# Kernel optimization log

Hardware: AMD Instinct MI355X
Metric: run time of the kernel (lower is better)

The kernel has to match this reference:

```python
import jax, jax.numpy as jnp
import numpy as np

N, B, E, H, D, L, NT = 30000, 16, 60000, 128, 64, 2, 5


def _build_graph():
    rng = np.random.default_rng(0)
    ng = N // B
    row = rng.integers(0, N, size=E)
    g = row // ng
    col = g * ng + rng.integers(0, ng, size=E)  # bonds stay within a graph
    order = np.argsort(g, kind='stable')        # sort bonds by graph id
    row, col = row[order], col[order]
    edge_index = np.stack([row, col]).astype(np.int32)
    # bond graph: bonds adjacent iff they share an atom (vectorized _build_bond_graph)
    atoms = np.concatenate([row, col])
    bonds = np.concatenate([np.arange(E), np.arange(E)])
    o2 = np.argsort(atoms, kind='stable')
    sb = bonds[o2]
    counts = np.bincount(atoms, minlength=N)
    offs = np.concatenate([[0], np.cumsum(counts)[:-1]])
    sq = counts * counts
    total = int(sq.sum())
    gid = np.repeat(np.arange(N), sq)
    poff = np.concatenate([[0], np.cumsum(sq)[:-1]])
    pos = np.arange(total) - np.repeat(poff, sq)
    c, o = counts[gid], offs[gid]
    ii, jj = pos // c, pos % c
    mask = ii != jj
    bond_edge_index = np.stack([sb[o + ii][mask], sb[o + jj][mask]]).astype(np.int32)
    batch = np.repeat(np.arange(B), ng).astype(np.int32)
    return edge_index, bond_edge_index, batch


def setup_inputs() -> dict:
    edge_index, bond_edge_index, batch = _build_graph()
    key = jax.random.key(0)
    ks = jax.random.split(key, 16)
    s = 0.05
    n = lambda k, shp: jax.random.normal(k, shp, jnp.float32) * s
    return {
        'atom_features': jax.random.normal(ks[0], (N, H), jnp.float32),
        'atom_pos': jax.random.normal(ks[1], (N, 3), jnp.float32),
        'atomic_numbers': jax.random.randint(ks[2], (N,), 1, 20, jnp.int32),
        'batch': jnp.asarray(batch),
        'edge_index': jnp.asarray(edge_index),
        'bond_edge_index': jnp.asarray(bond_edge_index),
        'iw1': n(ks[3], (2 * H, D)), 'ib1': jnp.zeros((D,), jnp.float32),
        'iw2': n(ks[4], (D, D)), 'ib2': jnp.zeros((D,), jnp.float32),
        'emb': n(ks[5], (L, NT, D)),
        'mw1': n(ks[6], (L, 3 * D, D)), 'mb1': jnp.zeros((L, D), jnp.float32),
        'mw2': n(ks[7], (L, D, D)), 'mb2': jnp.zeros((L, D), jnp.float32),
        'uw1': n(ks[8], (L, 2 * D, D)), 'ub1': jnp.zeros((L, D), jnp.float32),
        'uw2': n(ks[9], (L, D, D)), 'ub2': jnp.zeros((L, D), jnp.float32),
        'num_graphs': B,
    }


def reference(atom_features, atom_pos, iw1, ib1, iw2, ib2, emb, mw1, mb1, mw2, mb2,
              uw1, ub1, uw2, ub2, atomic_numbers, batch, edge_index, bond_edge_index,
              num_graphs):
    row, col = edge_index
    hi, hj = atom_features[row], atom_features[col]  # [E, H] gathers
    # bond_init MLP
    x = jax.nn.silu(jnp.concatenate([hi, hj], -1) @ iw1 + ib1) @ iw2 + ib2  # [E, D]
    # _classify_bonds: cosine-similarity thresholds (order matters, matches torch)
    ni = jnp.maximum(jnp.linalg.norm(hi, axis=-1), 1e-8)
    nj = jnp.maximum(jnp.linalg.norm(hj, axis=-1), 1e-8)
    sim = jnp.sum(hi * hj, -1) / (ni * nj)
    bt = jnp.where(sim > 0.8, 1, 0)
    bt = jnp.where(sim > 0.9, 2, bt)
    bt = jnp.where(sim < 0.3, 3, bt)
    src, dst = bond_edge_index  # x_j = x[src], x_i = x[dst]; aggregate at dst
    nb = x.shape[0]
    deg = jax.ops.segment_sum(jnp.ones(src.shape, jnp.float32), dst, num_segments=nb)
    denom = jnp.maximum(deg, 1.0)[:, None]  # PyG mean aggr: 0 for isolated nodes
    for l in range(mw1.shape[0]):
        te = emb[l][bt]  # [E, D] bond-type embedding
        msg_in = jnp.concatenate([x[dst], x[src], te[dst]], -1)  # [BE, 3D]
        msg = jax.nn.silu(msg_in @ mw1[l] + mb1[l]) @ mw2[l] + mb2[l]
        aggr = jax.ops.segment_sum(msg, dst, num_segments=nb) / denom
        upd_in = jnp.concatenate([aggr, x], -1)
        x = x + jax.nn.silu(upd_in @ uw1[l] + ub1[l]) @ uw2[l] + ub2[l]
    # pooling: edges are sorted by graph, so repeat_interleave == batch[row]
    bond_batch = batch[row]
    cnt = jax.ops.segment_sum(jnp.ones((nb,), jnp.float32), bond_batch, num_segments=num_graphs)
    gfeat = jax.ops.segment_sum(x, bond_batch, num_segments=num_graphs) / jnp.maximum(cnt, 1.0)[:, None]
    return x, gfeat
```

## Files before the change

kernel.cpp:

```cpp
#include <hip/hip_runtime.h>
#include <hip/hip_cooperative_groups.h>
#include <cstdint>
#include <cstddef>

namespace cg = cooperative_groups;

#define HDIM 128
#define DDIM 64
#define NTYPES 5
#define NGRAPHS 16
#define EPB 64
#define SCAP 1024
#define PREPB 132

typedef __attribute__((ext_vector_type(8))) short short8;
typedef __attribute__((ext_vector_type(4))) float f32x4;

static __device__ __forceinline__ short8 as_s8(uint4 u) {
    return __builtin_bit_cast(short8, u);
}

static __device__ __forceinline__ float silu_f(float v) {
    return v * __builtin_amdgcn_rcpf(1.0f + __expf(-v));
}
// ... 221 lines not shown
    const float* __restrict__ emb, const float* __restrict__ mw1,
    const float* __restrict__ mb1, const float* __restrict__ mw2,
    const float* __restrict__ mb2, const float* __restrict__ uw1,
    const float* __restrict__ uw2, const float* __restrict__ iw2,
    const float* __restrict__ iw1,
    float* __restrict__ tt, float* __restrict__ b2u,
    uint4* __restrict__ fw2u, uint4* __restrict__ fu1b, uint4* __restrict__ fu2,
    uint4* __restrict__ fp, uint4* __restrict__ fiw2, uint4* __restrict__ fp0,
    uint4* __restrict__ fiw1, int* __restrict__ cnt, int E) {
    for (int i = blockIdx.x * 256 + threadIdx.x; i < E; i += gridDim.x * 256)
        cnt[i] = 0;
    if (threadIdx.x < 64)
        dev_prep(blockIdx.x, threadIdx.x, emb, mw1, mb1, mw2, mb2, uw1, uw2, iw2, iw1,
                 tt, b2u, fw2u, fu1b, fu2, fp, fiw2, fp0, fiw1);
}

static __device__ __forceinline__ int slotIdx(int row, int slot) {
    return row * 8 + (slot ^ (row & 7));
}
static __device__ __forceinline__ int slotIdx16(int row, int slot) {
    return row * 16 + (slot ^ (row & 7));
}

static __device__ __forceinline__ short8 ldFragA(const uint4* buf, int rowBase, int lane, int ks) {
    int row = rowBase + (lane & 15);
    int slot = ks * 4 + (lane >> 4);
    return as_s8(buf[slotIdx(row, slot)]);
}
static __device__ __forceinline__ short8 ldFragA16(const uint4* buf, int rowBase, int lane, int slot0) {
    int row = rowBase + (lane & 15);
    int slot = slot0 + (lane >> 4);
    return as_s8(buf[slotIdx16(row, slot)]);
}

static __device__ __forceinline__ void loadB(const uint4* __restrict__ frag, int jt, int lane,
                                             short8& h0, short8& h1, short8& l0, short8& l1) {
    const uint4* p0 = frag + ((size_t)(jt * 2 + 0) * 64 + lane) * 2;
    const uint4* p1 = frag + ((size_t)(jt * 2 + 1) * 64 + lane) * 2;
    h0 = as_s8(p0[0]); l0 = as_s8(p0[1]);
    h1 = as_s8(p1[0]); l1 = as_s8(p1[1]);
}

static __device__ __forceinline__ f32x4 gemm_tile(const uint4* Ahi, const uint4* Alo,
        int rowBase, int lane,
        short8 bh0, short8 bh1, short8 bl0, short8 bl1, f32x4 acc) {
    short8 ah0 = ldFragA(Ahi, rowBase, lane, 0);
    short8 ah1 = ldFragA(Ahi, rowBase, lane, 1);
    short8 al0 = ldFragA(Alo, rowBase, lane, 0);
    short8 al1 = ldFragA(Alo, rowBase, lane, 1);
    acc = __builtin_amdgcn_mfma_f32_16x16x32_bf16(ah0, bh0, acc, 0, 0, 0);
    acc = __builtin_amdgcn_mfma_f32_16x16x32_bf16(ah1, bh1, acc, 0, 0, 0);
    acc = __builtin_amdgcn_mfma_f32_16x16x32_bf16(al0, bh0, acc, 0, 0, 0);
    acc = __builtin_amdgcn_mfma_f32_16x16x32_bf16(al1, bh1, acc, 0, 0, 0);
    acc = __builtin_amdgcn_mfma_f32_16x16x32_bf16(ah0, bl0, acc, 0, 0, 0);
    acc = __builtin_amdgcn_mfma_f32_16x16x32_bf16(ah1, bl1, acc, 0, 0, 0);
    return acc;
}

static __device__ __forceinline__ f32x4 gemm_tile16(const uint4* Ahi, const uint4* Alo,
        int rowBase, int lane, int sb,
        short8 bh0, short8 bh1, short8 bl0, short8 bl1, f32x4 acc) {
    short8 ah0 = ldFragA16(Ahi, rowBase, lane, sb + 0);
    short8 ah1 = ldFragA16(Ahi, rowBase, lane, sb + 4);
    short8 al0 = ldFragA16(Alo, rowBase, lane, sb + 0);
    short8 al1 = ldFragA16(Alo, rowBase, lane, sb + 4);
    acc = __builtin_amdgcn_mfma_f32_16x16x32_bf16(ah0, bh0, acc, 0, 0, 0);
    acc = __builtin_amdgcn_mfma_f32_16x16x32_bf16(ah1, bh1, acc, 0, 0, 0);
    acc = __builtin_amdgcn_mfma_f32_16x16x32_bf16(al0, bh0, acc, 0, 0, 0);
    acc = __builtin_amdgcn_mfma_f32_16x16x32_bf16(al1, bh1, acc, 0, 0, 0);
    acc = __builtin_amdgcn_mfma_f32_16x16x32_bf16(ah0, bl0, acc, 0, 0, 0);
    acc = __builtin_amdgcn_mfma_f32_16x16x32_bf16(ah1, bl1, acc, 0, 0, 0);
    return acc;
}

static __device__ __forceinline__ void dev_atom_proj(
    int a0, int tid, int lane, int w,
    const float* __restrict__ AF, const uint4* __restrict__ fIw1,
    float* __restrict__ pa, float* __restrict__ qa, float* __restrict__ na, int N,
    uint4* sHi, uint4* sLo) {
    {
        int dl = tid >> 3, q = tid & 7;
        int a = a0 + dl;
        bool ok = a < N;
        const float* ar = AF + (size_t)(ok ? a : 0) * HDIM + q * 16;
        float4 v0 = ld4(ar + 0), v1 = ld4(ar + 4), v2 = ld4(ar + 8), v3 = ld4(ar + 12);
        float nrm = v0.x*v0.x + v0.y*v0.y + v0.z*v0.z + v0.w*v0.w
                  + v1.x*v1.x + v1.y*v1.y + v1.z*v1.z + v1.w*v1.w
                  + v2.x*v2.x + v2.y*v2.y + v2.z*v2.z + v2.w*v2.w
                  + v3.x*v3.x + v3.y*v3.y + v3.z*v3.z + v3.w*v3.w;
        nrm += __shfl_xor(nrm, 1, 64);
        nrm += __shfl_xor(nrm, 2, 64);
        nrm += __shfl_xor(nrm, 4, 64);
        if (q == 0 && ok) na[a] = sqrtf(nrm);
        float f0[8] = {v0.x, v0.y, v0.z, v0.w, v1.x, v1.y, v1.z, v1.w};
        float f1[8] = {v2.x, v2.y, v2.z, v2.w, v3.x, v3.y, v3.z, v3.w};
        if (!ok) {
            #pragma unroll
            for (int i = 0; i < 8; ++i) { f0[i] = 0.f; f1[i] = 0.f; }
        }
        uint4 h, l;
        hilo8(f0, h, l);
        int s0 = slotIdx16(dl, q * 2);
        sHi[s0] = h; sLo[s0] = l;
        hilo8(f1, h, l);
        int s1 = slotIdx16(dl, q * 2 + 1);
        sHi[s1] = h; sLo[s1] = l;
    }
    int jt = w & 3;
    const uint4* m0 = fIw1 + ((w < 4) ? 0 : 2048);
    short8 B0h0, B0h1, B0l0, B0l1, B1h0, B1h1, B1l0, B1l1;
    loadB(m0, jt, lane, B0h0, B0h1, B0l0, B0l1);
    loadB(m0 + 1024, jt, lane, B1h0, B1h1, B1l0, B1l1);
    __syncthreads();

    float* dst = (w < 4) ? pa : qa;
    int j = jt * 16 + (lane & 15);
    f32x4 z4 = {0.f, 0.f, 0.f, 0.f};
    #pragma unroll
    for (int rt = 0; rt < 4; ++rt) {
        f32x4 acc = gemm_tile16(sHi, sLo, rt * 16, lane, 0, B0h0, B0h1, B0l0, B0l1, z4);
        acc = gemm_tile16(sHi, sLo, rt * 16, lane, 8, B1h0, B1h1, B1l0, B1l1, acc);
        #pragma unroll
        for (int r = 0; r < 4; ++r) {
            int rowi = rt * 16 + (lane >> 4) * 4 + r;
            int a = a0 + rowi;
            if (a < N) dst[(size_t)a * DDIM + j] = acc[r];
        }
    }
}

__global__ void __launch_bounds__(512) atom_proj_k(
    const float* __restrict__ AF, const uint4* __restrict__ fIw1,
    float* __restrict__ pa, float* __restrict__ qa, float* __restrict__ na, int N) {
    __shared__ uint4 sHi[1024];
    __shared__ uint4 sLo[1024];
    int tid = threadIdx.x, lane = tid & 63;
    int w = __builtin_amdgcn_readfirstlane((int)(tid >> 6));
    int a0 = blockIdx.x * 64;
    if (a0 < N)
        dev_atom_proj(a0, tid, lane, w, AF, fIw1, pa, qa, na, N, sHi, sLo);
}

static __device__ __forceinline__ void dev_bond_init(
    int lb, int tid, int lane, int w,
    const float* __restrict__ AF, const int* __restrict__ row, const int* __restrict__ col,
    const float* __restrict__ pa, const float* __restrict__ qa, const float* __restrict__ na,
    const float* __restrict__ b1, const uint4* __restrict__ fW2, const float* __restrict__ b2,
    const uint4* __restrict__ fP0,
    float* __restrict__ x, int* __restrict__ bt,
    float* __restrict__ pd, uint4* __restrict__ ps, int E,
    uint4* sAhi, uint4* sAlo, uint4* sXhi, uint4* sXlo, bool storeX) {
    int e0 = lb * EPB;

    {
        int dl = tid >> 3, q = tid & 7;
        int d = e0 + dl;
        bool ok = d < E;
        int dd = ok ? d : 0;
        int r = row[dd], c = col[dd];
        int jq = q * 8;

        const float* hi = AF + (size_t)r * HDIM + q * 16;
        const float* hj = AF + (size_t)c * HDIM + q * 16;
        float dt = 0.f;
        #pragma unroll
        for (int k = 0; k < 16; k += 4) {
            float4 a4 = ld4(hi + k), b4 = ld4(hj + k);
            dt += a4.x * b4.x + a4.y * b4.y + a4.z * b4.z + a4.w * b4.w;
        }
        dt += __shfl_xor(dt, 1, 64);
        dt += __shfl_xor(dt, 2, 64);
        dt += __shfl_xor(dt, 4, 64);
        if (q == 0 && ok) {
            float nr = fmaxf(na[r], 1e-8f), nc = fmaxf(na[c], 1e-8f);
            float sim = dt / (nr * nc);
            int t = 0;
            if (sim > 0.8f) t = 1;
            if (sim > 0.9f) t = 2;
            if (sim < 0.3f) t = 3;
            bt[d] = t;
        }

        const float* pr = pa + (size_t)r * DDIM + jq;
        const float* qc = qa + (size_t)c * DDIM + jq;
        float4 p0 = ld4(pr + 0), p1 = ld4(pr + 4);
        float4 q0 = ld4(qc + 0), q1 = ld4(qc + 4);
        float hv[8];
        hv[0] = silu_f(p0.x + q0.x + b1[jq + 0]);
        hv[1] = silu_f(p0.y + q0.y + b1[jq + 1]);
        hv[2] = silu_f(p0.z + q0.z + b1[jq + 2]);
        hv[3] = silu_f(p0.w + q0.w + b1[jq + 3]);
        hv[4] = silu_f(p1.x + q1.x + b1[jq + 4]);
        hv[5] = silu_f(p1.y + q1.y + b1[jq + 5]);
        hv[6] = silu_f(p1.z + q1.z + b1[jq + 6]);
        hv[7] = silu_f(p1.w + q1.w + b1[jq + 7]);
        if (!ok) {
            #pragma unroll
            for (int i = 0; i < 8; ++i) hv[i] = 0.f;
        }
        uint4 h4, l4;
        hilo8(hv, h4, l4);
        int si = slotIdx(dl, q);
        sAhi[si] = h4; sAlo[si] = l4;
    }
    int jt = w & 3, mh = w >> 2;
    short8 W2h0, W2h1, W2l0, W2l1;
    loadB(fW2, jt, lane, W2h0, W2h1, W2l0, W2l1);
    __syncthreads();

    int rb0 = mh * 32, rb1 = mh * 32 + 16;
    f32x4 z4 = {0.f, 0.f, 0.f, 0.f};
    f32x4 acc0 = gemm_tile(sAhi, sAlo, rb0, lane, W2h0, W2h1, W2l0, W2l1, z4);
    f32x4 acc1 = gemm_tile(sAhi, sAlo, rb1, lane, W2h0, W2h1, W2l0, W2l1, z4);
    int j = jt * 16 + (lane & 15);
    float b2j = b2[j];
    unsigned short* hX = (unsigned short*)sXhi;
    unsigned short* lX = (unsigned short*)sXlo;
    #pragma unroll
    for (int r = 0; r < 4; ++r) {
        int rowi = rb0 + (lane >> 4) * 4 + r;
        int e = e0 + rowi;
        float xn = acc0[r] + b2j;
        if (storeX && e < E) x[(size_t)e * DDIM + j] = xn;
        unsigned int hb = bf16r(xn);
        float lov = xn - __uint_as_float(hb << 16);
        int ui = (rowi * 8 + ((j >> 3) ^ (rowi & 7))) * 8 + (j & 7);
        hX[ui] = (unsigned short)hb;
        lX[ui] = (unsigned short)bf16r(lov);
    }
    #pragma unroll
    for (int r = 0; r < 4; ++r) {
        int rowi = rb1 + (lane >> 4) * 4 + r;
        int e = e0 + rowi;
        float xn = acc1[r] + b2j;
        if (storeX && e < E) x[(size_t)e * DDIM + j] = xn;
        unsigned int hb = bf16r(xn);
        float lov = xn - __uint_as_float(hb << 16);
        int ui = (rowi * 8 + ((j >> 3) ^ (rowi & 7))) * 8 + (j & 7);
        hX[ui] = (unsigned short)hb;
        lX[ui] = (unsigned short)bf16r(lov);
    }
    __syncthreads();

    const uint4* fPw = (w < 4) ? fP0 : (fP0 + 1024);
    int jp = w & 3;
    short8 Ph0, Ph1, Pl0, Pl1;
    loadB(fPw, jp, lane, Ph0, Ph1, Pl0, Pl1);
    f32x4 q0 = gemm_tile(sXhi, sXlo, 0,  lane, Ph0, Ph1, Pl0, Pl1, z4);
    f32x4 q1 = gemm_tile(sXhi, sXlo, 16, lane, Ph0, Ph1, Pl0, Pl1, z4);
    f32x4 q2 = gemm_tile(sXhi, sXlo, 32, lane, Ph0, Ph1, Pl0, Pl1, z4);
    f32x4 q3 = gemm_tile(sXhi, sXlo, 48, lane, Ph0, Ph1, Pl0, Pl1, z4);
    unsigned short* hA = (unsigned short*)sAhi;
    if (w < 4) {
        int jd = jp * 16 + (lane & 15);
        #pragma unroll
        for (int mt = 0; mt < 4; ++mt) {
            f32x4 qq = (mt == 0) ? q0 : (mt == 1) ? q1 : (mt == 2) ? q2 : q3;
            #pragma unroll
            for (int r = 0; r < 4; ++r) {
                int rowi = mt * 16 + (lane >> 4) * 4 + r;
                int e = e0 + rowi;
                if (e < E) pd[(size_t)e * DDIM + jd] = qq[r];
            }
        }
    } else {
        int js = jp * 16 + (lane & 15);
        #pragma unroll
        for (int mt = 0; mt < 4; ++mt) {
            f32x4 qq = (mt == 0) ? q0 : (mt == 1) ? q1 : (mt == 2) ? q2 : q3;
            #pragma unroll
            for (int r = 0; r < 4; ++r) {
                int rowi = mt * 16 + (lane >> 4) * 4 + r;
                int ui = (rowi * 8 + ((js >> 3) ^ (rowi & 7))) * 8 + (js & 7);
                hA[ui] = (unsigned short)bf16r(qq[r]);
            }
        }
    }
    __syncthreads();
    {
        int dl = tid >> 3, q = tid & 7;
        int d = e0 + dl;
        if (d < E) ps[(size_t)d * 8 + q] = sAhi[slotIdx(dl, q)];
    }
}

__global__ void __launch_bounds__(512, 4) bond_init2_k(
    const float* __restrict__ AF, const int* __restrict__ row, const int* __restrict__ col,
    const float* __restrict__ pa, const float* __restrict__ qa, const float* __restrict__ na,
    const float* __restrict__ b1, const uint4* __restrict__ fW2, const float* __restrict__ b2,
    const uint4* __restrict__ fP0,
    float* __restrict__ x, int* __restrict__ bt,
    float* __restrict__ pd, uint4* __restrict__ ps, int E) {
    __shared__ uint4 sAhi[512];
    __shared__ uint4 sAlo[512];
    __shared__ uint4 sXhi[512];
    __shared__ uint4 sXlo[512];
    int nEB = (E + EPB - 1) / EPB;
    int lb = xcd_logical_block();
    if (lb >= nEB) return;
    int tid = threadIdx.x, lane = tid & 63;
    int w = __builtin_amdgcn_readfirstlane((int)(tid >> 6));
    dev_bond_init(lb, tid, lane, w, AF, row, col, pa, qa, na, b1, fW2, b2, fP0,
                  x, bt, pd, ps, E, sAhi, sAlo, sXhi, sXlo, true);
}

__global__ void __launch_bounds__(256) proj_k(const float* __restrict__ x,
                                              const float* __restrict__ w1 ,
                                              float* __restrict__ pd, uint4* __restrict__ ps,
                                              int E) {
    int lane = threadIdx.x & 63;
    int w = __builtin_amdgcn_readfirstlane((int)(threadIdx.x >> 6));
    int e = blockIdx.x * EPB + lane;
    bool ok = e < E;
    int eidx = ok ? e : 0;
    int j0 = w * 16;
    const float* xr = x + (size_t)eidx * DDIM;

    float apd[16], aps[16];
    #pragma unroll
    for (int jj = 0; jj < 16; ++jj) { apd[jj] = 0.f; aps[jj] = 0.f; }
    #pragma unroll 2
    for (int c = 0; c < 16; ++c) {
        float4 v = ld4(xr + c * 4);
        float xv[4] = {v.x, v.y, v.z, v.w};
        #pragma unroll
        for (int kk = 0; kk < 4; ++kk) {
            int k = c * 4 + kk;
            const float* wd = w1 + (size_t)k * DDIM + j0;
            const float* wsv = w1 + (size_t)(DDIM + k) * DDIM + j0;
            #pragma unroll
            for (int jj = 0; jj < 16; ++jj) {
                apd[jj] = fmaf(xv[kk], wd[jj], apd[jj]);
                aps[jj] = fmaf(xv[kk], wsv[jj], aps[jj]);
            }
        }
    }
    if (ok) {
        float* pr = pd + (size_t)e * DDIM + j0;
        st4(pr + 0,  make_float4(apd[0],  apd[1],  apd[2],  apd[3]));
        st4(pr + 4,  make_float4(apd[4],  apd[5],  apd[6],  apd[7]));
        st4(pr + 8,  make_float4(apd[8],  apd[9],  apd[10], apd[11]));
        st4(pr + 12, make_float4(apd[12], apd[13], apd[14], apd[15]));
        ps[(size_t)e * 8 + 2 * w + 0] = pack8(aps + 0);
        ps[(size_t)e * 8 + 2 * w + 1] = pack8(aps + 8);
    }
}

static __device__ __forceinline__ void dev_layer(
    int lb, int tid, int lane, int w,
    float* __restrict__ x, const float* __restrict__ pd, const uint4* __restrict__ ps,
    const float* __restrict__ tt_l, const int* __restrict__ bt,
    const int* __restrict__ offs, const int* __restrict__ srclist,
    const int* __restrict__ cnt,
    const uint4* __restrict__ fW2u, const float* __restrict__ b2u,
    const uint4* __restrict__ fU1b, const float* __restrict__ ub1,
    const uint4* __restrict__ fU2, const float* __restrict__ ub2,
    const uint4* __restrict__ fP, float* __restrict__ pdn, uint4* __restrict__ psn,
    int E, const int* __restrict__ erow, const int* __restrict__ gbatch,
    float* __restrict__ gfeat, int doPool,
    uint4* sAhi, uint4* sAlo, uint4* sXhi, uint4* sXlo,
    float* degLDS, int* gidLDS, int* sIdx, bool loadX, bool storeX3) {
    int e0 = lb * EPB;
    int pb0 = offs[e0];

    {
        int dl = tid >> 3, q = tid & 7;
        int d = e0 + dl;
        bool ok = d < E;
        int dd = ok ? d : 0;
        int jq = q * 8;
        float4 xv0 = make_float4(0, 0, 0, 0), xv1 = xv0;
        if (loadX) {
            const float* xr = x + (size_t)dd * DDIM + jq;
            xv0 = ld4(xr + 0); xv1 = ld4(xr + 4);
        }
        int dc = cnt[dd];
        int rAtom = (doPool && ok) ? erow[dd] : 0;
        const float* pr = pd + (size_t)dd * DDIM + jq;
        const float* tp = tt_l + (size_t)bt[dd] * DDIM + jq;
        float4 b0 = add4(ld4(pr + 0), ld4(tp + 0));
        float4 b1 = add4(ld4(pr + 4), ld4(tp + 4));
        int p0v = ok ? offs[d] : pb0, p1v = ok ? offs[d + 1] : pb0;

        int emax = min(e0 + EPB, E);
        int pT = offs[emax] - pb0;
        for (int i = tid; i < pT && i < SCAP; i += 512) sIdx[i] = srclist[pb0 + i];
        __syncthreads();

        float4 s0 = make_float4(0, 0, 0, 0), s1 = s0;
        if (p1v - pb0 <= SCAP) {
            int li = p0v - pb0, le = p1v - pb0;
            for (; li + 4 <= le; li += 4) {
                uint4 u0 = ps[(size_t)sIdx[li + 0] * 8 + q];
                uint4 u1 = ps[(size_t)sIdx[li + 1] * 8 + q];
                uint4 u2 = ps[(size_t)sIdx[li + 2] * 8 + q];
                uint4 u3 = ps[(size_t)sIdx[li + 3] * 8 + q];
                float4 a, b;
                unpack8(u0, a, b);
                silu_acc4(s0, add4(b0, a));
                silu_acc4(s1, add4(b1, b));
                unpack8(u1, a, b);
                silu_acc4(s0, add4(b0, a));
                silu_acc4(s1, add4(b1, b));
                unpack8(u2, a, b);
                silu_acc4(s0, add4(b0, a));
                silu_acc4(s1, add4(b1, b));
                unpack8(u3, a, b);
                silu_acc4(s0, add4(b0, a));
                silu_acc4(s1, add4(b1, b));
            }
            for (; li < le; ++li) {
                uint4 u0 = ps[(size_t)sIdx[li] * 8 + q];
                float4 a, b;
                unpack8(u0, a, b);
                silu_acc4(s0, add4(b0, a));
                silu_acc4(s1, add4(b1, b));
            }
        } else {
            int p = p0v;
            for (; p + 4 <= p1v; p += 4) {
                uint4 u0 = ps[(size_t)srclist[p + 0] * 8 + q];
                uint4 u1 = ps[(size_t)srclist[p + 1] * 8 + q];
                uint4 u2 = ps[(size_t)srclist[p + 2] * 8 + q];
                uint4 u3 = ps[(size_t)srclist[p + 3] * 8 + q];
                float4 a, b;
                unpack8(u0, a, b);
                silu_acc4(s0, add4(b0, a));
                silu_acc4(s1, add4(b1, b));
                unpack8(u1, a, b);
                silu_acc4(s0, add4(b0, a));
                silu_acc4(s1, add4(b1, b));
                unpack8(u2, a, b);
                silu_acc4(s0, add4(b0, a));
                silu_acc4(s1, add4(b1, b));
                unpack8(u3, a, b);
                silu_acc4(s0, add4(b0, a));
                silu_acc4(s1, add4(b1, b));
            }
            for (; p < p1v; ++p) {
                uint4 u0 = ps[(size_t)srclist[p] * 8 + q];
                float4 a, b;
                unpack8(u0, a, b);
                silu_acc4(s0, add4(b0, a));
                silu_acc4(s1, add4(b1, b));
            }
        }
        float inv = 1.0f / fmaxf((float)dc, 1.0f);
        float sv[8] = {s0.x * inv, s0.y * inv, s0.z * inv, s0.w * inv,
                       s1.x * inv, s1.y * inv, s1.z * inv, s1.w * inv};
        if (!ok) {
            #pragma unroll
            for (int i = 0; i < 8; ++i) sv[i] = 0.f;
        }
        uint4 h4, l4;
        int si = slotIdx(dl, q);
        hilo8(sv, h4, l4);
        sAhi[si] = h4; sAlo[si] = l4;
        if (loadX) {
            float xf[8] = {xv0.x, xv0.y, xv0.z, xv0.w, xv1.x, xv1.y, xv1.z, xv1.w};
            if (!ok) {
                #pragma unroll
                for (int i = 0; i < 8; ++i) xf[i] = 0.f;
            }
            hilo8(xf, h4, l4);
            sXhi[si] = h4; sXlo[si] = l4;
        }
        if (q == 0) {
            degLDS[dl] = (ok && dc > 0) ? 1.0f : 0.0f;
            gidLDS[dl] = (doPool && ok) ? gbatch[rAtom] : -1;
        }
    }
    int jt = w & 3, mh = w >> 2;
    short8 A2h0, A2h1, A2l0, A2l1;
    short8 U1h0, U1h1, U1l0, U1l1;
    loadB(fW2u, jt, lane, A2h0, A2h1, A2l0, A2l1);
    loadB(fU1b, jt, lane, U1h0, U1h1, U1l0, U1l1);
    __syncthreads();

    int rb0 = mh * 32, rb1 = mh * 32 + 16;
    f32x4 z4 = {0.f, 0.f, 0.f, 0.f};
    f32x4 acc0 = z4, acc1 = z4;
    acc0 = gemm_tile(sAhi, sAlo, rb0, lane, A2h0, A2h1, A2l0, A2l1, acc0);
    acc0 = gemm_tile(sXhi, sXlo, rb0, lane, U1h0, U1h1, U1l0, U1l1, acc0);
    acc1 = gemm_tile(sAhi, sAlo, rb1, lane, A2h0, A2h1, A2l0, A2l1, acc1);
    acc1 = gemm_tile(sXhi, sXlo, rb1, lane, U1h0, U1h1, U1l0, U1l1, acc1);
    __syncthreads();
    int j = jt * 16 + (lane & 15);
    float ub1j = ub1[j], b2uj = b2u[j];
    unsigned short* hA = (unsigned short*)sAhi;
    unsigned short* lA = (unsigned short*)sAlo;
    #pragma unroll
    for (int r = 0; r < 4; ++r) {
        int row = rb0 + (lane >> 4) * 4 + r;
        float hv = silu_f(acc0[r] + ub1j + degLDS[row] * b2uj);
        unsigned int hb = bf16r(hv);
        float lov = hv - __uint_as_float(hb << 16);
        int ui = (row * 8 + ((j >> 3) ^ (row & 7))) * 8 + (j & 7);
        hA[ui] = (unsigned short)hb;
        lA[ui] = (unsigned short)bf16r(lov);
    }
    #pragma unroll
    for (int r = 0; r < 4; ++r) {
        int row = rb1 + (lane >> 4) * 4 + r;
        float hv = silu_f(acc1[r] + ub1j + degLDS[row] * b2uj);
        unsigned int hb = bf16r(hv);
        float lov = hv - __uint_as_float(hb << 16);
        int ui = (row * 8 + ((j >> 3) ^ (row & 7))) * 8 + (j & 7);
        hA[ui] = (unsigned short)hb;
        lA[ui] = (unsigned short)bf16r(lov);
    }
    __syncthreads();

    short8 U2h0, U2h1, U2l0, U2l1;
    loadB(fU2, jt, lane, U2h0, U2h1, U2l0, U2l1);
    f32x4 o0 = gemm_tile(sAhi, sAlo, rb0, lane, U2h0, U2h1, U2l0, U2l1, z4);
    f32x4 o1 = gemm_tile(sAhi, sAlo, rb1, lane, U2h0, U2h1, U2l0, U2l1, z4);
    float ub2j = ub2[j];
    bool haveP = (fP != nullptr);
    unsigned short* hX = (unsigned short*)sXhi;
    unsigned short* lX = (unsigned short*)sXlo;
    float xnv0[4], xnv1[4];
    #pragma unroll
    for (int r = 0; r < 4; ++r) {
        int row = rb0 + (lane >> 4) * 4 + r;
        int e = e0 + row;
        int ui = (row * 8 + ((j >> 3) ^ (row & 7))) * 8 + (j & 7);
        float xvv = __uint_as_float((unsigned int)hX[ui] << 16)
                  + __uint_as_float((unsigned int)lX[ui] << 16);
        float xn = xvv + o0[r] + ub2j;
        xnv0[r] = xn;
        if (storeX3 && e < E) x[(size_t)e * DDIM + j] = xn;
        if (haveP) {
            unsigned int hb = bf16r(xn);
            float lov = xn - __uint_as_float(hb << 16);
            hX[ui] = (unsigned short)hb;
            lX[ui] = (unsigned short)bf16r(lov);
        }
    }
    #pragma unroll
    for (int r = 0; r < 4; ++r) {
        int row = rb1 + (lane >> 4) * 4 + r;
        int e = e0 + row;
        int ui = (row * 8 + ((j >> 3) ^ (row & 7))) * 8 + (j & 7);
        float xvv = __uint_as_float((unsigned int)hX[ui] << 16)
                  + __uint_as_float((unsigned int)lX[ui] << 16);
        float xn = xvv + o1[r] + ub2j;
        xnv1[r] = xn;
        if (storeX3 && e < E) x[(size_t)e * DDIM + j] = xn;
        if (haveP) {
            unsigned int hb = bf16r(xn);
            float lov = xn - __uint_as_float(hb << 16);
            hX[ui] = (unsigned short)hb;
            lX[ui] = (unsigned short)bf16r(lov);
        }
    }
    if (!haveP) {
        if (doPool) {
            __syncthreads();
            float* poolB = (float*)sAhi;
            if (tid < 256) poolB[tid] = 0.f;
            __syncthreads();
            int gid0 = gidLDS[0];
            bool uni = (gidLDS[EPB - 1] == gid0);
            if (uni) {
                float s = xnv0[0] + xnv0[1] + xnv0[2] + xnv0[3]
                        + xnv1[0] + xnv1[1] + xnv1[2] + xnv1[3];
                atomicAdd(&poolB[j], s);
            } else {
                #pragma unroll
                for (int r = 0; r < 4; ++r) {
                    int row = rb0 + (lane >> 4) * 4 + r;
                    int g = gidLDS[row];
                    if (g >= 0) {
                        int sl = g - gid0;
                        if (sl < 4) atomicAdd(&poolB[sl * DDIM + j], xnv0[r]);
                        else atomicAdd(&gfeat[(size_t)g * DDIM + j], xnv0[r]);
                    }
                }
                #pragma unroll
                for (int r = 0; r < 4; ++r) {
                    int row = rb1 + (lane >> 4) * 4 + r;
                    int g = gidLDS[row];
                    if (g >= 0) {
                        int sl = g - gid0;
                        if (sl < 4) atomicAdd(&poolB[sl * DDIM + j], xnv1[r]);
                        else atomicAdd(&gfeat[(size_t)g * DDIM + j], xnv1[r]);
                    }
                }
            }
            __syncthreads();
            if (tid < 256) {
                int sl = tid >> 6;
                int g = gid0 + sl;
                float v = poolB[tid];
                if (v != 0.f && g < NGRAPHS)
                    atomicAdd(&gfeat[(size_t)g * DDIM + (tid & 63)], v);
            }
        }
        return;
    }
    __syncthreads();

    const uint4* fPw = (w < 4) ? fP : (fP + 1024);
    int jp = w & 3;
    short8 Ph0, Ph1, Pl0, Pl1;
    loadB(fPw, jp, lane, Ph0, Ph1, Pl0, Pl1);
    f32x4 q0 = gemm_tile(sXhi, sXlo, 0,  lane, Ph0, Ph1, Pl0, Pl1, z4);
    f32x4 q1 = gemm_tile(sXhi, sXlo, 16, lane, Ph0, Ph1, Pl0, Pl1, z4);
    f32x4 q2 = gemm_tile(sXhi, sXlo, 32, lane, Ph0, Ph1, Pl0, Pl1, z4);
    f32x4 q3 = gemm_tile(sXhi, sXlo, 48, lane, Ph0, Ph1, Pl0, Pl1, z4);
    if (w < 4) {
        int jd = jp * 16 + (lane & 15);
        #pragma unroll
        for (int mt = 0; mt < 4; ++mt) {
            f32x4 qq = (mt == 0) ? q0 : (mt == 1) ? q1 : (mt == 2) ? q2 : q3;
            #pragma unroll
            for (int r = 0; r < 4; ++r) {
                int row = mt * 16 + (lane >> 4) * 4 + r;
                int e = e0 + row;
                if (e < E) pdn[(size_t)e * DDIM + jd] = qq[r];
            }
        }
    } else {
        int js = jp * 16 + (lane & 15);
        #pragma unroll
        for (int mt = 0; mt < 4; ++mt) {
            f32x4 qq = (mt == 0) ? q0 : (mt == 1) ? q1 : (mt == 2) ? q2 : q3;
            #pragma unroll
            for (int r = 0; r < 4; ++r) {
                int row = mt * 16 + (lane >> 4) * 4 + r;
                int ui = (row * 8 + ((js >> 3) ^ (row & 7))) * 8 + (js & 7);
                hA[ui] = (unsigned short)bf16r(qq[r]);
            }
        }
    }
    __syncthreads();
    {
        int dl = tid >> 3, q = tid & 7;
        int d = e0 + dl;
        if (d < E) psn[(size_t)d * 8 + q] = sAhi[slotIdx(dl, q)];
    }
}

__global__ void __launch_bounds__(512, 4) layer_k(
    float* __restrict__ x, const float* __restrict__ pd, const uint4* __restrict__ ps,
    const float* __restrict__ tt_l, const int* __restrict__ bt,
    const int* __restrict__ offs, const int* __restrict__ srclist,
    const int* __restrict__ cnt,
    const uint4* __restrict__ fW2u, const float* __restrict__ b2u,
    const uint4* __restrict__ fU1b, const float* __restrict__ ub1,
    const uint4* __restrict__ fU2, const float* __restrict__ ub2,
    const uint4* __restrict__ fP,
    float* __restrict__ pdn, uint4* __restrict__ psn, int E,
    const int* __restrict__ erow, const int* __restrict__ gbatch,
    float* __restrict__ gfeat, int doPool) {
    __shared__ uint4 sAhi[512];
    __shared__ uint4 sAlo[512];
    __shared__ uint4 sXhi[512];
    __shared__ uint4 sXlo[512];
    __shared__ float degLDS[64];
    __shared__ int   gidLDS[64];
    __shared__ int   sIdx[SCAP];
    int nEB = (E + EPB - 1) / EPB;
    int lb = xcd_logical_block();
    if (lb >= nEB) return;
    int tid = threadIdx.x, lane = tid & 63;
    int w = __builtin_amdgcn_readfirstlane((int)(tid >> 6));
    dev_layer(lb, tid, lane, w, x, pd, ps, tt_l, bt, offs, srclist, cnt,
              fW2u, b2u, fU1b, ub1, fU2, ub2, fP, pdn, psn, E,
              erow, gbatch, gfeat, doPool,
              sAhi, sAlo, sXhi, sXlo, degLDS, gidLDS, sIdx, true, true);
}

static __device__ __forceinline__ int lower_bound_bb(const int* __restrict__ row,
                                                     const int* __restrict__ batch,
                                                     int E, int g) {
    int lo = 0, hi = E;
    while (lo < hi) {
        int m = (lo + hi) >> 1;
        if (batch[row[m]] < g) lo = m + 1; else hi = m;
    }
    return lo;
}

__global__ void __launch_bounds__(64) pool_final_k(
    const int* __restrict__ row, const int* __restrict__ batch,
    float* __restrict__ gfeat, int E) {
    int g = blockIdx.x, j = threadIdx.x;
    int s = lower_bound_bb(row, batch, E, g);
    int t = lower_bound_bb(row, batch, E, g + 1);
    float cnt = fmaxf((float)(t - s), 1.0f);
    gfeat[g * DDIM + j] /= cnt;
}

__global__ void __launch_bounds__(512, 8) fused_k(
    float* x, const int* row, const int* col,
    const float* AF, const uint4* fIw1, float* pa, float* qa, float* na, int N,
    const float* ib1, const uint4* fIw2, const float* ib2, const uint4* fP0,
    int* bt, float* pd, uint4* ps,
    const float* tt, int* offs, int* srclist, int* cnt,
    const uint4* fW2u, const float* b2u, const uint4* fU1b, const float* ub1,
    const uint4* fU2, const float* ub2, const uint4* fP,
    float* pd2, uint4* ps2,
    const int* gbatch, float* gfeat, int E,
    const int* bsrc, const int* bdst, int BE,
    int* bsum, int* bpre, int* cursor) {
    __shared__ uint4 U1[1024];
    __shared__ uint4 U2[1024];
    __shared__ float degLDS[64];
    __shared__ int   gidLDS[64];
    __shared__ int   sIdx[SCAP];
    cg::grid_group grid = cg::this_grid();
    int tid = threadIdx.x, lane = tid & 63;
    int w = __builtin_amdgcn_readfirstlane((int)(tid >> 6));
    uint4* sAhi = U1;
    uint4* sAlo = U1 + 512;
    uint4* sXhi = U2;
    uint4* sXlo = U2 + 512;
    int nEB = (E + EPB - 1) / EPB;
    int lb = xcd_logical_block();

    if ((int)blockIdx.x * 64 < N)
        dev_atom_proj((int)blockIdx.x * 64, tid, lane, w, AF, fIw1, pa, qa, na, N, U1, U2);
    for (int i = (int)blockIdx.x * 512 + tid; i < BE; i += (int)gridDim.x * 512)
        __hip_atomic_fetch_add(&cnt[bdst[i]], 1, __ATOMIC_RELAXED, __HIP_MEMORY_SCOPE_AGENT);
    if (blockIdx.x == gridDim.x - 1)
        for (int i = tid; i < NGRAPHS * DDIM; i += 512) gfeat[i] = 0.f;
    __threadfence();
    grid.sync();

    if (lb < nEB) {
        dev_bond_init(lb, tid, lane, w, AF, row, col, pa, qa, na, ib1, fIw2, ib2, fP0,
                      x, bt, pd, ps, E, sAhi, sAlo, sXhi, sXlo, false);
        if (tid < 64) {
            int e = lb * EPB + tid;
            int v = (e < E) ? cnt[e] : 0;
            v += __shfl_xor(v, 1, 64);
            v += __shfl_xor(v, 2, 64);
            v += __shfl_xor(v, 4, 64);
            v += __shfl_xor(v, 8, 64);
            v += __shfl_xor(v, 16, 64);
            v += __shfl_xor(v, 32, 64);
            if (tid == 0) bsum[lb] = v;
        }
    }
    __threadfence();
    grid.sync();

    if (blockIdx.x == 0) {
        for (int i = tid; i < SCAP; i += 512) sIdx[i] = (i < nEB) ? bsum[i] : 0;
        __syncthreads();
        for (int off = 1; off < SCAP; off <<= 1) {
            int i2 = tid + 512;
            int v0 = (tid >= off) ? sIdx[tid - off] : 0;
            int v1 = sIdx[i2 - off];
            __syncthreads();
            sIdx[tid] += v0;
            sIdx[i2] += v1;
            __syncthreads();
        }
        for (int i = tid; i < nEB; i += 512) bpre[i] = sIdx[i] - bsum[i];
    }
    __threadfence();
    grid.sync();

    if (lb < nEB) {
        int e0 = lb * EPB;
        int myc = 0;
        if (tid < 64) {
            int e = e0 + tid;
            myc = (e < E) ? cnt[e] : 0;
            gidLDS[tid] = myc;
        }
        __syncthreads();
        for (int off = 1; off < 64; off <<= 1) {
            int v = 0;
            if (tid < 64 && tid >= off) v = gidLDS[tid - off];
            __syncthreads();
            if (tid < 64) gidLDS[tid] += v;
            __syncthreads();
        }
        if (tid < 64) {
            int e = e0 + tid;
            if (e < E) {
                int ex = gidLDS[tid] - myc + bpre[lb];
                offs[e] = ex;
                cursor[e] = ex;
                if (e == E - 1) offs[E] = ex + myc;
            }
        }
    }
    __threadfence();
    grid.sync();

    for (int i = (int)blockIdx.x * 512 + tid; i < BE; i += (int)gridDim.x * 512) {
        int d = bdst[i];
        int p = __hip_atomic_fetch_add(&cursor[d], 1, __ATOMIC_RELAXED,
                                       __HIP_MEMORY_SCOPE_AGENT);
        srclist[p] = bsrc[i];
    }
    __threadfence();
    grid.sync();

    if (lb < nEB)
        dev_layer(lb, tid, lane, w, x, pd, ps, tt, bt, offs, srclist, cnt,
                  fW2u, b2u, fU1b, ub1, fU2, ub2, fP, pd2, ps2, E,
                  row, gbatch, gfeat, 0,
                  sAhi, sAlo, sXhi, sXlo, degLDS, gidLDS, sIdx, false, false);
    __threadfence();
    grid.sync();

    if (lb < nEB)
        dev_layer(lb, tid, lane, w, x, pd2, ps2, tt + NTYPES * DDIM, bt, offs, srclist, cnt,
                  fW2u + 1024, b2u + DDIM, fU1b + 1024, ub1 + DDIM,
                  fU2 + 1024, ub2 + DDIM, nullptr, nullptr, nullptr, E,
                  row, gbatch, gfeat, 1,
                  sAhi, sAlo, sXhi, sXlo, degLDS, gidLDS, sIdx, false, true);
    __threadfence();
    grid.sync();

    if ((int)blockIdx.x < NGRAPHS && tid < 64) {
        int g = blockIdx.x, j = tid;
        int s = lower_bound_bb(row, gbatch, E, g);
        int t = lower_bound_bb(row, gbatch, E, g + 1);
        float c = fmaxf((float)(t - s), 1.0f);
        gfeat[g * DDIM + j] /= c;
    }
}

extern "C" void kernel_launch(void* const* d_in, const int* in_sizes, int n_in,
                              void* d_out, int out_size, void* d_ws, size_t ws_size,
                              hipStream_t stream) {
    (void)n_in; (void)out_size;
    const float* AF    = (const float*)d_in[0];
    const int*   batch = (const int*)d_in[3];
    const int*   edge_index      = (const int*)d_in[4];
    const int*   bond_edge_index = (const int*)d_in[5];
    const float* iw1 = (const float*)d_in[6];
    const float* ib1 = (const float*)d_in[7];
    const float* iw2 = (const float*)d_in[8];
    const float* ib2 = (const float*)d_in[9];
    const float* emb = (const float*)d_in[10];
    const float* mw1 = (const float*)d_in[11];
    const float* mb1 = (const float*)d_in[12];
    const float* mw2 = (const float*)d_in[13];
    const float* mb2 = (const float*)d_in[14];
    const float* uw1 = (const float*)d_in[15];
    const float* ub1 = (const float*)d_in[16];
    const float* uw2 = (const float*)d_in[17];
    const float* ub2 = (const float*)d_in[18];

    const int N  = in_sizes[0] / HDIM;
    const int E  = in_sizes[4] / 2;
    const int BE = in_sizes[5] / 2;
    const int NB = (E + 255) / 256;
    const int EB = (E + EPB - 1) / EPB;
    const int nEB = EB;
    const int APB = (N + 63) / 64;
    const int EBS = ((EB + 7) / 8) * 8;
    const int CNTB = (BE + 255) / 256;

    float* xout  = (float*)d_out;
    float* gfeat = xout + (size_t)E * DDIM;

    char* w = (char*)d_ws;
    float* tt       = (float*)w;  w += sizeof(float) * 2 * NTYPES * DDIM;
    float* b2u      = (float*)w;  w += sizeof(float) * 2 * DDIM;
    w = (char*)(((uintptr_t)w + 15) & ~(uintptr_t)15);
    uint4* fW2u     = (uint4*)w;  w += 2048 * sizeof(uint4);
    uint4* fU1b     = (uint4*)w;  w += 2048 * sizeof(uint4);
    uint4* fU2      = (uint4*)w;  w += 2048 * sizeof(uint4);
    uint4* fP       = (uint4*)w;  w += 2048 * sizeof(uint4);
    uint4* fIw2     = (uint4*)w;  w += 1024 * sizeof(uint4);
    uint4* fP0      = (uint4*)w;  w += 2048 * sizeof(uint4);
    uint4* fIw1     = (uint4*)w;  w += 4096 * sizeof(uint4);
    int*   cnt      = (int*)w;    w += sizeof(int) * E;
    int*   offs     = (int*)w;    w += sizeof(int) * (E + 1);
    int*   cursor   = (int*)w;    w += sizeof(int) * E;
    int*   bt       = (int*)w;    w += sizeof(int) * E;
    int*   srclist  = (int*)w;    w += sizeof(int) * BE;
    int*   bsum     = (int*)w;    w += sizeof(int) * 1024;
    int*   bpre     = (int*)w;    w += sizeof(int) * 1024;
    w = (char*)(((uintptr_t)w + 15) & ~(uintptr_t)15);
    float* pd       = (float*)w;  w += sizeof(float) * (size_t)E * DDIM;
    uint4* ps       = (uint4*)w;  w += sizeof(unsigned short) * (size_t)E * DDIM;
    float* pa       = (float*)w;  w += sizeof(float) * (size_t)N * DDIM;
    float* qa       = (float*)w;  w += sizeof(float) * (size_t)N * DDIM;
    float* na       = (float*)w;  w += sizeof(float) * (size_t)N;
    w = (char*)(((uintptr_t)w + 15) & ~(uintptr_t)15);
    float* pd2      = (float*)w;  w += sizeof(float) * (size_t)E * DDIM;
    uint4* ps2      = (uint4*)w;  w += sizeof(unsigned short) * (size_t)E * DDIM;
    bool fuse_proj = ((size_t)(w - (char*)d_ws) <= ws_size);

    const int* row  = edge_index;
    const int* col  = edge_index + E;
    const int* bsrc = bond_edge_index;
    const int* bdst = bond_edge_index + BE;

    prep_k<<<PREPB, 256, 0, stream>>>(emb, mw1, mb1, mw2, mb2, uw1, uw2, iw2, iw1,
                                      tt, b2u, fW2u, fU1b, fU2, fP, fIw2, fP0, fIw1,
                                      cnt, E);

    static int s_coopBlocks = -1;
    if (s_coopBlocks < 0) {
        int dev = 0;
        hipGetDevice(&dev);
        int coopAttr = 0;
        hipDeviceGetAttribute(&coopAttr, hipDeviceAttributeCooperativeLaunch, dev);
        int nCU = 0;
        hipDeviceGetAttribute(&nCU, hipDeviceAttributeMultiprocessorCount, dev);
        int mb = 0;
        hipError_t oe = hipOccupancyMaxActiveBlocksPerMultiprocessor(&mb, fused_k, 512, 0);
        s_coopBlocks = (coopAttr && oe == hipSuccess && nCU > 0) ? mb * nCU : 0;
    }

    bool coopDone = false;
    if (fuse_proj && s_coopBlocks >= EBS && nEB <= SCAP) {
        int Nv = N, Ev = E, BEv = BE;
        void* kargs[] = {
            (void*)&xout, (void*)&row, (void*)&col,
            (void*)&AF, (void*)&fIw1, (void*)&pa, (void*)&qa, (void*)&na, (void*)&Nv,
            (void*)&ib1, (void*)&fIw2, (void*)&ib2, (void*)&fP0,
            (void*)&bt, (void*)&pd, (void*)&ps,
            (void*)&tt, (void*)&offs, (void*)&srclist, (void*)&cnt,
            (void*)&fW2u, (void*)&b2u, (void*)&fU1b, (void*)&ub1,
            (void*)&fU2, (void*)&ub2, (void*)&fP,
            (void*)&pd2, (void*)&ps2,
            (void*)&batch, (void*)&gfeat, (void*)&Ev,
            (void*)&bsrc, (void*)&bdst, (void*)&BEv,
            (void*)&bsum, (void*)&bpre, (void*)&cursor };
        hipError_t le = hipLaunchCooperativeKernel((const void*)fused_k, dim3(EBS),
                                                   dim3(512), kargs, 0, stream);
        coopDone = (le == hipSuccess);
    }

    if (!coopDone) {
        count_k<<<CNTB, 256, 0, stream>>>(bdst, cnt, BE);
        bsum_k<<<NB, 256, 0, stream>>>(cnt, bsum, E);
        bscan_k<<<1, 1024, 0, stream>>>(bsum, bpre, NB);
        offs_k<<<NB, 256, 0, stream>>>(cnt, bpre, offs, cursor, E);
        scatter_k<<<(BE + 255) / 256, 256, 0, stream>>>(bsrc, bdst, cursor, srclist, BE);
        atom_proj_k<<<APB, 512, 0, stream>>>(AF, fIw1, pa, qa, na, N);
        bond_init2_k<<<EBS, 512, 0, stream>>>(AF, row, col, pa, qa, na, ib1, fIw2, ib2,
                                              fP0, xout, bt, pd, ps, E);
        hipMemsetAsync(gfeat, 0, NGRAPHS * DDIM * sizeof(float), stream);
        if (fuse_proj) {
            layer_k<<<EBS, 512, 0, stream>>>(
                xout, pd, ps, tt, bt, offs, srclist, cnt,
                fW2u, b2u, fU1b, ub1, fU2, ub2,
                fP, pd2, ps2, E, row, batch, gfeat, 0);
            layer_k<<<EBS, 512, 0, stream>>>(
                xout, pd2, ps2, tt + NTYPES * DDIM, bt, offs, srclist, cnt,
                fW2u + 1024, b2u + DDIM, fU1b + 1024, ub1 + DDIM,
                fU2 + 1024, ub2 + DDIM,
                nullptr, nullptr, nullptr, E, row, batch, gfeat, 1);
        } else {
            for (int l = 0; l < 2; ++l) {
                if (l > 0)
                    proj_k<<<EB, 256, 0, stream>>>(xout, mw1 + (size_t)l * 192 * 64, pd, ps, E);
                layer_k<<<EBS, 512, 0, stream>>>(
                    xout, pd, ps, tt + (size_t)l * NTYPES * DDIM, bt, offs, srclist, cnt,
                    fW2u + (size_t)l * 1024, b2u + (size_t)l * DDIM,
                    fU1b + (size_t)l * 1024, ub1 + (size_t)l * DDIM,
                    fU2 + (size_t)l * 1024, ub2 + (size_t)l * DDIM,
                    nullptr, nullptr, nullptr, E, row, batch, gfeat, l == 1 ? 1 : 0);
            }
        }
        pool_final_k<<<NGRAPHS, 64, 0, stream>>>(row, batch, gfeat, E);
    }
}
```

Measured before the change: 280.6 us.

## Fold weight prep into cooperative kernel and replace global scan with per-block prefix sums

Moves the weight-preparation and count-zeroing work from a separate prep_k launch into a new first phase of the cooperative fused kernel. It also removes one grid-wide barrier: each block now sums the preceding block totals itself with an LDS tree reduction, instead of block 0 running a single scan followed by a grid sync. This saves a kernel launch and a grid.sync. The cost is an extra grid.sync at the start and redundant O(nEB) reads of bsum in every block. The unused proj_k path is deleted.

```diff
diff --git a/kernel.cpp b/kernel.cpp
--- a/kernel.cpp
+++ b/kernel.cpp
@@ -547,48 +547,6 @@
     int w = __builtin_amdgcn_readfirstlane((int)(tid >> 6));
     dev_bond_init(lb, tid, lane, w, AF, row, col, pa, qa, na, b1, fW2, b2, fP0,
                   x, bt, pd, ps, E, sAhi, sAlo, sXhi, sXlo, true);
-}
-
-__global__ void __launch_bounds__(256) proj_k(const float* __restrict__ x,
-                                              const float* __restrict__ w1 ,
-                                              float* __restrict__ pd, uint4* __restrict__ ps,
-                                              int E) {
-    int lane = threadIdx.x & 63;
-    int w = __builtin_amdgcn_readfirstlane((int)(threadIdx.x >> 6));
-    int e = blockIdx.x * EPB + lane;
-    bool ok = e < E;
-    int eidx = ok ? e : 0;
-    int j0 = w * 16;
-    const float* xr = x + (size_t)eidx * DDIM;
-
-    float apd[16], aps[16];
-    #pragma unroll
-    for (int jj = 0; jj < 16; ++jj) { apd[jj] = 0.f; aps[jj] = 0.f; }
-    #pragma unroll 2
-    for (int c = 0; c < 16; ++c) {
-        float4 v = ld4(xr + c * 4);
-        float xv[4] = {v.x, v.y, v.z, v.w};
-        #pragma unroll
-        for (int kk = 0; kk < 4; ++kk) {
-            int k = c * 4 + kk;
-            const float* wd = w1 + (size_t)k * DDIM + j0;
-            const float* wsv = w1 + (size_t)(DDIM + k) * DDIM + j0;
-            #pragma unroll
-            for (int jj = 0; jj < 16; ++jj) {
-                apd[jj] = fmaf(xv[kk], wd[jj], apd[jj]);
-                aps[jj] = fmaf(xv[kk], wsv[jj], aps[jj]);
-            }
-        }
-    }
-    if (ok) {
-        float* pr = pd + (size_t)e * DDIM + j0;
-        st4(pr + 0,  make_float4(apd[0],  apd[1],  apd[2],  apd[3]));
-        st4(pr + 4,  make_float4(apd[4],  apd[5],  apd[6],  apd[7]));
-        st4(pr + 8,  make_float4(apd[8],  apd[9],  apd[10], apd[11]));
-        st4(pr + 12, make_float4(apd[12], apd[13], apd[14], apd[15]));
-        ps[(size_t)e * 8 + 2 * w + 0] = pack8(aps + 0);
-        ps[(size_t)e * 8 + 2 * w + 1] = pack8(aps + 8);
-    }
 }
 
 static __device__ __forceinline__ void dev_layer(
@@ -940,16 +898,22 @@
 
 __global__ void __launch_bounds__(512, 8) fused_k(
     float* x, const int* row, const int* col,
-    const float* AF, const uint4* fIw1, float* pa, float* qa, float* na, int N,
-    const float* ib1, const uint4* fIw2, const float* ib2, const uint4* fP0,
+    const float* AF, float* pa, float* qa, float* na, int N,
+    const float* ib1, const float* ib2,
     int* bt, float* pd, uint4* ps,
-    const float* tt, int* offs, int* srclist, int* cnt,
-    const uint4* fW2u, const float* b2u, const uint4* fU1b, const float* ub1,
-    const uint4* fU2, const float* ub2, const uint4* fP,
+    int* offs, int* srclist, int* cnt,
+    const float* b2uc, const float* ub1, const float* ub2,
     float* pd2, uint4* ps2,
     const int* gbatch, float* gfeat, int E,
     const int* bsrc, const int* bdst, int BE,
-    int* bsum, int* bpre, int* cursor) {
+    int* bsum, int* cursor,
+    const float* emb, const float* mw1, const float* mb1,
+    const float* mw2, const float* mb2, const float* uw1,
+    const float* uw2, const float* iw2, const float* iw1,
+    float* tt, float* b2u,
+    uint4* fW2u, uint4* fU1b, uint4* fU2, uint4* fP,
+    uint4* fIw2, uint4* fP0, uint4* fIw1) {
+    (void)b2uc;
     __shared__ uint4 U1[1024];
     __shared__ uint4 U2[1024];
     __shared__ float degLDS[64];
@@ -965,6 +929,14 @@
     int nEB = (E + EPB - 1) / EPB;
     int lb = xcd_logical_block();
 
+    for (int i = (int)blockIdx.x * 512 + tid; i < E; i += (int)gridDim.x * 512)
+        cnt[i] = 0;
+    if ((int)blockIdx.x < PREPB && tid < 64)
+        dev_prep((int)blockIdx.x, tid, emb, mw1, mb1, mw2, mb2, uw1, uw2, iw2, iw1,
+                 tt, b2u, fW2u, fU1b, fU2, fP, fIw2, fP0, fIw1);
+    __threadfence();
+    grid.sync();
+
     if ((int)blockIdx.x * 64 < N)
         dev_atom_proj((int)blockIdx.x * 64, tid, lane, w, AF, fIw1, pa, qa, na, N, U1, U2);
     for (int i = (int)blockIdx.x * 512 + tid; i < BE; i += (int)gridDim.x * 512)
@@ -992,24 +964,18 @@
     __threadfence();
     grid.sync();
 
-    if (blockIdx.x == 0) {
-        for (int i = tid; i < SCAP; i += 512) sIdx[i] = (i < nEB) ? bsum[i] : 0;
+    if (lb < nEB) {
+        int s = 0;
+        for (int i = tid; i < lb; i += 512) s += bsum[i];
+        sIdx[tid] = s;
         __syncthreads();
-        for (int off = 1; off < SCAP; off <<= 1) {
-            int i2 = tid + 512;
-            int v0 = (tid >= off) ? sIdx[tid - off] : 0;
-            int v1 = sIdx[i2 - off];
+        #pragma unroll
+        for (int off2 = 256; off2 > 0; off2 >>= 1) {
+            if (tid < off2) sIdx[tid] += sIdx[tid + off2];
             __syncthreads();
-            sIdx[tid] += v0;
-            sIdx[i2] += v1;
-            __syncthreads();
-        }
-        for (int i = tid; i < nEB; i += 512) bpre[i] = sIdx[i] - bsum[i];
-    }
-    __threadfence();
-    grid.sync();
-
-    if (lb < nEB) {
+        }
+        int bpreL = sIdx[0];
+        __syncthreads();
         int e0 = lb * EPB;
         int myc = 0;
         if (tid < 64) {
@@ -1028,7 +994,7 @@
         if (tid < 64) {
             int e = e0 + tid;
             if (e < E) {
-                int ex = gidLDS[tid] - myc + bpre[lb];
+                int ex = gidLDS[tid] - myc + bpreL;
                 offs[e] = ex;
                 cursor[e] = ex;
                 if (e == E - 1) offs[E] = ex + myc;
@@ -1142,10 +1108,6 @@
     const int* bsrc = bond_edge_index;
     const int* bdst = bond_edge_index + BE;
 
-    prep_k<<<PREPB, 256, 0, stream>>>(emb, mw1, mb1, mw2, mb2, uw1, uw2, iw2, iw1,
-                                      tt, b2u, fW2u, fU1b, fU2, fP, fIw2, fP0, fIw1,
-                                      cnt, E);
-
     static int s_coopBlocks = -1;
     if (s_coopBlocks < 0) {
         int dev = 0;
@@ -1164,22 +1126,30 @@
         int Nv = N, Ev = E, BEv = BE;
         void* kargs[] = {
             (void*)&xout, (void*)&row, (void*)&col,
-            (void*)&AF, (void*)&fIw1, (void*)&pa, (void*)&qa, (void*)&na, (void*)&Nv,
-            (void*)&ib1, (void*)&fIw2, (void*)&ib2, (void*)&fP0,
+            (void*)&AF, (void*)&pa, (void*)&qa, (void*)&na, (void*)&Nv,
+            (void*)&ib1, (void*)&ib2,
             (void*)&bt, (void*)&pd, (void*)&ps,
-            (void*)&tt, (void*)&offs, (void*)&srclist, (void*)&cnt,
-            (void*)&fW2u, (void*)&b2u, (void*)&fU1b, (void*)&ub1,
-            (void*)&fU2, (void*)&ub2, (void*)&fP,
+            (void*)&offs, (void*)&srclist, (void*)&cnt,
+            (void*)&b2u, (void*)&ub1, (void*)&ub2,
             (void*)&pd2, (void*)&ps2,
             (void*)&batch, (void*)&gfeat, (void*)&Ev,
             (void*)&bsrc, (void*)&bdst, (void*)&BEv,
-            (void*)&bsum, (void*)&bpre, (void*)&cursor };
+            (void*)&bsum, (void*)&cursor,
+            (void*)&emb, (void*)&mw1, (void*)&mb1,
+            (void*)&mw2, (void*)&mb2, (void*)&uw1,
+            (void*)&uw2, (void*)&iw2, (void*)&iw1,
+            (void*)&tt, (void*)&b2u,
+            (void*)&fW2u, (void*)&fU1b, (void*)&fU2, (void*)&fP,
+            (void*)&fIw2, (void*)&fP0, (void*)&fIw1 };
         hipError_t le = hipLaunchCooperativeKernel((const void*)fused_k, dim3(EBS),
                                                    dim3(512), kargs, 0, stream);
         coopDone = (le == hipSuccess);
     }
 
     if (!coopDone) {
+        prep_k<<<PREPB, 256, 0, stream>>>(emb, mw1, mb1, mw2, mb2, uw1, uw2, iw2, iw1,
+                                          tt, b2u, fW2u, fU1b, fU2, fP, fIw2, fP0, fIw1,
+                                          cnt, E);
         count_k<<<CNTB, 256, 0, stream>>>(bdst, cnt, BE);
         bsum_k<<<NB, 256, 0, stream>>>(cnt, bsum, E);
         bscan_k<<<1, 1024, 0, stream>>>(bsum, bpre, NB);
@@ -1189,28 +1159,15 @@
         bond_init2_k<<<EBS, 512, 0, stream>>>(AF, row, col, pa, qa, na, ib1, fIw2, ib2,
                                               fP0, xout, bt, pd, ps, E);
         hipMemsetAsync(gfeat, 0, NGRAPHS * DDIM * sizeof(float), stream);
-        if (fuse_proj) {
-            layer_k<<<EBS, 512, 0, stream>>>(
-                xout, pd, ps, tt, bt, offs, srclist, cnt,
-                fW2u, b2u, fU1b, ub1, fU2, ub2,
-                fP, pd2, ps2, E, row, batch, gfeat, 0);
-            layer_k<<<EBS, 512, 0, stream>>>(
-                xout, pd2, ps2, tt + NTYPES * DDIM, bt, offs, srclist, cnt,
-                fW2u + 1024, b2u + DDIM, fU1b + 1024, ub1 + DDIM,
-                fU2 + 1024, ub2 + DDIM,
-                nullptr, nullptr, nullptr, E, row, batch, gfeat, 1);
-        } else {
-            for (int l = 0; l < 2; ++l) {
-                if (l > 0)
-                    proj_k<<<EB, 256, 0, stream>>>(xout, mw1 + (size_t)l * 192 * 64, pd, ps, E);
-                layer_k<<<EBS, 512, 0, stream>>>(
-                    xout, pd, ps, tt + (size_t)l * NTYPES * DDIM, bt, offs, srclist, cnt,
-                    fW2u + (size_t)l * 1024, b2u + (size_t)l * DDIM,
-                    fU1b + (size_t)l * 1024, ub1 + (size_t)l * DDIM,
-                    fU2 + (size_t)l * 1024, ub2 + (size_t)l * DDIM,
-                    nullptr, nullptr, nullptr, E, row, batch, gfeat, l == 1 ? 1 : 0);
-            }
-        }
+        layer_k<<<EBS, 512, 0, stream>>>(
+            xout, pd, ps, tt, bt, offs, srclist, cnt,
+            fW2u, b2u, fU1b, ub1, fU2, ub2,
+            fP, pd2, ps2, E, row, batch, gfeat, 0);
+        layer_k<<<EBS, 512, 0, stream>>>(
+            xout, pd2, ps2, tt + NTYPES * DDIM, bt, offs, srclist, cnt,
+            fW2u + 1024, b2u + DDIM, fU1b + 1024, ub1 + DDIM,
+            fU2 + 1024, ub2 + DDIM,
+            nullptr, nullptr, nullptr, E, row, batch, gfeat, 1);
         pool_final_k<<<NGRAPHS, 64, 0, stream>>>(row, batch, gfeat, E);
     }
 }
```

Measured after the change: 284.2 us. Within noise of the previous version (+1.3%).
